# Performance work log

Hardware: AMD Instinct MI355X
Metric: run time of the kernel (lower is better)

Reference implementation:

```python
import jax, jax.numpy as jnp
import numpy as np

S, B, E = 2048, 2, 1024
H = 16
HD = E // H
RANK = 8
ALPHA = 16.0
LORA_SCALE = ALPHA / RANK


def setup_inputs() -> dict:
    key = jax.random.key(0)
    ks = jax.random.split(key, 13)
    d = {
        'query': jax.random.normal(ks[0], (S, B, E), jnp.float32),
        'key': jax.random.normal(ks[1], (S, B, E), jnp.float32),
        'value': jax.random.normal(ks[2], (S, B, E), jnp.float32),
        'in_proj_weight': jax.random.normal(ks[3], (3 * E, E), jnp.float32) * 0.02,
        'in_proj_bias': jax.random.normal(ks[4], (3 * E,), jnp.float32) * 0.02,
        'out_w': jax.random.normal(ks[5], (E, E), jnp.float32) * 0.02,
        'out_b': jax.random.normal(ks[6], (E,), jnp.float32) * 0.02,
        'A_q': jax.random.normal(ks[7], (RANK, E), jnp.float32) * 0.02,
        'B_q': jax.random.normal(ks[8], (E, RANK), jnp.float32) * 0.02,
        'A_k': jax.random.normal(ks[9], (RANK, E), jnp.float32) * 0.02,
        'B_k': jax.random.normal(ks[10], (E, RANK), jnp.float32) * 0.02,
        'A_v': jax.random.normal(ks[11], (RANK, E), jnp.float32) * 0.02,
        'B_v': jax.random.normal(ks[12], (E, RANK), jnp.float32) * 0.02,
    }
    return d


def _proj(x, W, b, A, Bm):
    # frozen linear + LoRA low-rank delta: x @ W.T + b + ((x @ A.T) @ B.T) * scale
    base = jnp.einsum('sbe,fe->sbf', x, W) + b
    lora = jnp.einsum('sbr,fr->sbf', jnp.einsum('sbe,re->sbr', x, A), Bm) * LORA_SCALE
    return base + lora


def reference(query, key, value, in_proj_weight, in_proj_bias, out_w, out_b,
              A_q, B_q, A_k, B_k, A_v, B_v):
    Wq, Wk, Wv = in_proj_weight[:E], in_proj_weight[E:2 * E], in_proj_weight[2 * E:]
    bq, bk, bv = in_proj_bias[:E], in_proj_bias[E:2 * E], in_proj_bias[2 * E:]
    q = _proj(query, Wq, bq, A_q, B_q)   # [S,B,E]
    k = _proj(key, Wk, bk, A_k, B_k)
    v = _proj(value, Wv, bv, A_v, B_v)
    # reshape to [B*H, S, HD] (seq-first layout, matching torch view/transpose)
    def heads(x):
        return x.reshape(S, B * H, HD).transpose(1, 0, 2)
    qh, kh, vh = heads(q), heads(k), heads(v)
    scale = HD ** -0.5
    attn = jnp.einsum('nsd,ntd->nst', qh, kh) * scale  # [B*H,S,S]
    attn = jax.nn.softmax(attn, axis=-1)
    out = jnp.einsum('nst,ntd->nsd', attn, vh)         # [B*H,S,HD]
    out = out.transpose(1, 0, 2).reshape(S, B, E)
    out = jnp.einsum('sbe,fe->sbf', out, out_w) + out_b
    return out
```

## Files before the change

kernel.cpp:

```cpp
#include <hip/hip_runtime.h>
#include <stdint.h>

static const int S_ = 2048, B_ = 2, E_ = 1024, H_ = 16, HD_ = 64, MR_ = 4096;

typedef __bf16 bf16;
typedef __bf16 bf16x8 __attribute__((ext_vector_type(8)));
typedef float  f32x4  __attribute__((ext_vector_type(4)));
typedef float  f32x16 __attribute__((ext_vector_type(16)));
typedef unsigned short u16x8 __attribute__((ext_vector_type(8)));

#define AS1(p) ((const __attribute__((address_space(1))) void*)(p))
#define AS3(p) ((__attribute__((address_space(3))) void*)(p))

#define QSCALE 0.18033688011112042f

static __device__ __forceinline__ uint32_t cvtpk_bf16(float lo, float hi) {
    uint32_t r;
    asm("v_cvt_pk_bf16_f32 %0, %1, %2" : "=v"(r) : "v"(lo), "v"(hi));
    return r;
}

__global__ __launch_bounds__(256) void prep_all(const float* __restrict__ s0,
                                                const float* __restrict__ s1,
                                                const float* __restrict__ s2,
                                                const float* __restrict__ s3,
                                                bf16* __restrict__ d0,
                                                bf16* __restrict__ d1,
                                                bf16* __restrict__ d2,
                                                bf16* __restrict__ d3,
                                                const float* __restrict__ W,
                                                const float* __restrict__ A0,
                                                const float* __restrict__ B0,
                                                const float* __restrict__ A1,
                                                const float* __restrict__ B1,
                                                const float* __restrict__ A2,
                                                const float* __restrict__ B2,
                                                bf16* __restrict__ o0,
                                                bf16* __restrict__ o1,
                                                bf16* __restrict__ o2) {
    int b = blockIdx.x;
    if (b < 6656) {
        const float* src;
        bf16* dst;
        int i;
        if (b < 6144) {
            int seg = b >> 11;
            i = (b & 2047) * 256 + threadIdx.x;
            src = seg == 0 ? s0 : (seg == 1 ? s1 : s2);
            dst = seg == 0 ? d0 : (seg == 1 ? d1 : d2);
        } else {
            i = (b - 6144) * 256 + threadIdx.x;
            src = s3; dst = d3;
        }
        const float4* s = (const float4*)src;
        float4 a = s[i * 2], c = s[i * 2 + 1];
        bf16x8 v;
        v[0] = (bf16)a.x; v[1] = (bf16)a.y; v[2] = (bf16)a.z; v[3] = (bf16)a.w;
        v[4] = (bf16)c.x; v[5] = (bf16)c.y; v[6] = (bf16)c.z; v[7] = (bf16)c.w;
        *(bf16x8*)(dst + (size_t)i * 8) = v;
    } else {
        int bb = b - 6656;
        int z = bb >> 12;
        const float* A = z == 0 ? A0 : (z == 1 ? A1 : A2);
        const float* Bm = z == 0 ? B0 : (z == 1 ? B1 : B2);
        bf16* out = z == 0 ? o0 : (z == 1 ? o1 : o2);
        const float* Wz = W + (size_t)z * 1024 * 1024;
        int idx = (bb & 4095) * 256 + threadIdx.x;
        int f = idx >> 10, e = idx & 1023;
        float acc = Wz[idx];
#pragma unroll
        for (int r = 0; r < 8; r++) acc += 2.0f * Bm[f * 8 + r] * A[r * 1024 + e];
        out[idx] = (bf16)acc;
    }
}

__global__ __launch_bounds__(256) void gemm_qkv(const bf16* __restrict__ XQ,
                                                const bf16* __restrict__ XK,
                                                const bf16* __restrict__ XV,
                                                const bf16* __restrict__ WQ,
                                                const bf16* __restrict__ WK,
                                                const bf16* __restrict__ WV,
                                                const float* __restrict__ ipb,
                                                bf16* __restrict__ QH,
                                                bf16* __restrict__ KH,
                                                bf16* __restrict__ VH) {
    int z = blockIdx.z;
    const bf16* Amat = z == 0 ? XQ : (z == 1 ? XK : XV);
    const bf16* Bmat = z == 0 ? WQ : (z == 1 ? WK : WV);
    bf16* Cout = z == 0 ? QH : (z == 1 ? KH : VH);
    const float* bias = ipb + z * 1024;
    float cscale = z == 0 ? QSCALE : 1.0f;

    __shared__ bf16 smbuf[16896];
    const int tid = threadIdx.x;
    const int wid = tid >> 6, lane = tid & 63;
    const int lg = lane >> 4, li = lane & 15;
    const int bidl = blockIdx.y * 8 + blockIdx.x;
    const int orig = (bidl & 7) * 32 + (bidl >> 3);
    const int m0 = (orig >> 3) * 128, n0 = (orig & 7) * 128;
    const int wr = wid >> 1, wc = wid & 1;

    f32x4 acc[4][4] = {};

    for (int kt = 0; kt < 1024; kt += 64) {
        __syncthreads();
#pragma unroll
        for (int h = 0; h < 2; h++)
#pragma unroll
            for (int i = 0; i < 2; i++) {
                int c = wid * 2 + i;
                const bf16* ga = Amat + (size_t)(m0 + c * 16 + (lane >> 2)) * 1024 + kt + h * 32 + (lane & 3) * 8;
                __builtin_amdgcn_global_load_lds(AS1(ga), AS3(smbuf + h * 4096 + c * 512), 16, 0, 0);
                const bf16* gb = Bmat + (size_t)(n0 + c * 16 + (lane >> 2)) * 1024 + kt + h * 32 + (lane & 3) * 8;
                __builtin_amdgcn_global_load_lds(AS1(gb), AS3(smbuf + 8192 + h * 4096 + c * 512), 16, 0, 0);
            }
        __syncthreads();

#pragma unroll
        for (int h = 0; h < 2; h++) {
            bf16x8 a[4], b[4];
#pragma unroll
            for (int mi = 0; mi < 4; mi++)
                a[mi] = *(const bf16x8*)(smbuf + h * 4096 + (wr * 64 + mi * 16 + li) * 32 + lg * 8);
#pragma unroll
            for (int ni = 0; ni < 4; ni++)
                b[ni] = *(const bf16x8*)(smbuf + 8192 + h * 4096 + (wc * 64 + ni * 16 + li) * 32 + lg * 8);
#pragma unroll
            for (int mi = 0; mi < 4; mi++)
#pragma unroll
                for (int ni = 0; ni < 4; ni++)
                    acc[mi][ni] = __builtin_amdgcn_mfma_f32_16x16x32_bf16(a[mi], b[ni], acc[mi][ni], 0, 0, 0);
        }
    }

    __syncthreads();
#pragma unroll
    for (int ni = 0; ni < 4; ni++) {
        int fl = wc * 64 + ni * 16 + li;
        float bv = bias[n0 + fl];
#pragma unroll
        for (int mi = 0; mi < 4; mi++)
#pragma unroll
            for (int r = 0; r < 4; r++) {
                int ml_ = wr * 64 + mi * 16 + lg * 4 + r;
                smbuf[ml_ * 132 + fl] = (bf16)((acc[mi][ni][r] + bv) * cscale);
            }
    }
    __syncthreads();
#pragma unroll
    for (int k = 0; k < 8; k++) {
        int c = tid + 256 * k;
        int dhalf = c & 7, m = (c >> 3) & 127, hl = c >> 10;
        u16x8 v = *(const u16x8*)(smbuf + m * 132 + hl * 64 + dhalf * 8);
        int mg = m0 + m, fg = n0 + hl * 64;
        int s = mg >> 1, bb = mg & 1, h = fg >> 6, d = dhalf * 8;
        *(u16x8*)(Cout + (size_t)(bb * 16 + h) * S_ * 64 + (size_t)s * 64 + d) = v;
    }
}

__global__ __launch_bounds__(256) void gemm_out64(const bf16* __restrict__ Amat,
                                                  const bf16* __restrict__ Bmat,
                                                  const float* __restrict__ bias,
                                                  float* __restrict__ Cout) {
    __shared__ bf16 Asm[2][64 * 32];
    __shared__ bf16 Bsm[2][128 * 32];
    const int tid = threadIdx.x;
    const int wid = tid >> 6, lane = tid & 63;
    const int lg = lane >> 4, li = lane & 15;
    const int bidl = blockIdx.y * 8 + blockIdx.x;
    const int orig = (bidl & 7) * 64 + (bidl >> 3);
    const int m0 = (orig >> 3) * 64, n0 = (orig & 7) * 128;
    const int wr = wid >> 1, wc = wid & 1;

    f32x4 acc[2][4] = {};

    for (int kt = 0; kt < 1024; kt += 64) {
        __syncthreads();
#pragma unroll
        for (int h = 0; h < 2; h++)
            for (int j = wid; j < 12; j += 4) {
                if (j < 4) {
                    const bf16* ga = Amat + (size_t)(m0 + j * 16 + (lane >> 2)) * 1024 + kt + h * 32 + (lane & 3) * 8;
                    __builtin_amdgcn_global_load_lds(AS1(ga), AS3(&Asm[h][j * 512]), 16, 0, 0);
                } else {
                    int c = j - 4;
                    const bf16* gb = Bmat + (size_t)(n0 + c * 16 + (lane >> 2)) * 1024 + kt + h * 32 + (lane & 3) * 8;
                    __builtin_amdgcn_global_load_lds(AS1(gb), AS3(&Bsm[h][c * 512]), 16, 0, 0);
                }
            }
        __syncthreads();

#pragma unroll
        for (int h = 0; h < 2; h++) {
            bf16x8 a[2], b[4];
#pragma unroll
            for (int mi = 0; mi < 2; mi++)
                a[mi] = *(const bf16x8*)(&Asm[h][(wr * 32 + mi * 16 + li) * 32 + lg * 8]);
#pragma unroll
            for (int ni = 0; ni < 4; ni++)
                b[ni] = *(const bf16x8*)(&Bsm[h][(wc * 64 + ni * 16 + li) * 32 + lg * 8]);
#pragma unroll
            for (int mi = 0; mi < 2; mi++)
#pragma unroll
                for (int ni = 0; ni < 4; ni++)
                    acc[mi][ni] = __builtin_amdgcn_mfma_f32_16x16x32_bf16(a[mi], b[ni], acc[mi][ni], 0, 0, 0);
        }
    }

#pragma unroll
    for (int ni = 0; ni < 4; ni++) {
        int f = n0 + wc * 64 + ni * 16 + li;
        float bv = bias[f];
#pragma unroll
        for (int mi = 0; mi < 2; mi++)
#pragma unroll
            for (int r = 0; r < 4; r++) {
                int m = m0 + wr * 32 + mi * 16 + lg * 4 + r;
                Cout[(size_t)m * 1024 + f] = acc[mi][ni][r] + bv;
            }
    }
}

__global__ __launch_bounds__(256, 4) void attn_fwd(const bf16* __restrict__ qh,
                                                   const bf16* __restrict__ kh,
                                                   const bf16* __restrict__ vh,
                                                   bf16* __restrict__ outbuf) {
    __shared__ __attribute__((aligned(16))) char smem[32768];

    const int bid = blockIdx.x;
    const int head = (bid & 7) * 4 + ((bid >> 3) & 3);
    const int qt = bid >> 5;
    const int tid = threadIdx.x, wid = tid >> 6, l = tid & 63;
    const int li = l & 31, hi = l >> 5;
    const int kvh = wid & 1;

    const bf16* Qb = qh + (size_t)head * S_ * 64;
    const bf16* Kb = kh + (size_t)head * S_ * 64;
    const bf16* Vb = vh + (size_t)head * S_ * 64;
    const int q0 = qt * 64 + (wid >> 1) * 32;

    bf16x8 qf[4];
#pragma unroll
    for (int s = 0; s < 4; s++)
        qf[s] = *(const bf16x8*)(Qb + (size_t)(q0 + li) * 64 + 16 * s + 8 * hi);

    f32x16 oacc0 = {}, oacc1 = {};
    float lsum = 0.f;

    const size_t kg_off = ((size_t)(16 * (l & 7)) ^ (16 * ((l >> 3) & 7)));
    const int vk2 = tid & 31, vdb = (tid >> 5) * 8;
    const int rswz = 16 * (li & 7);

#define STAGE_K(kv0, dstbuf)                                                    \
    {                                                                           \
        _Pragma("unroll")                                                       \
        for (int j = 0; j < 2; j++) {                                           \
            int row = (j * 4 + wid) * 8 + (l >> 3);                             \
            const char* srcp = (const char*)Kb + (size_t)((kv0) + row) * 128 + kg_off; \
            __builtin_amdgcn_global_load_lds(AS1(srcp),                         \
                AS3((dstbuf) + (j * 4 + wid) * 1024), 16, 0, 0);                \
        }                                                                       \
    }

    u16x8 vreg0, vreg1;
    vreg0 = *(const u16x8*)(Vb + (size_t)(2 * vk2) * 64 + vdb);
    vreg1 = *(const u16x8*)(Vb + (size_t)(2 * vk2 + 1) * 64 + vdb);
    STAGE_K(0, smem);

    for (int t = 0; t < 32; t++) {
        const int cur = t & 1;
        char* Kc = smem + cur * 8192;
        char* Vc = smem + 16384 + cur * 8192;
#pragma unroll
        for (int i = 0; i < 8; i++) {
            uint32_t w = (uint32_t)vreg0[i] | ((uint32_t)vreg1[i] << 16);
            *(uint32_t*)(Vc + (vdb + i) * 128 + ((4 * vk2) ^ (16 * i))) = w;
        }
        __syncthreads();
        if (t + 1 < 32) {
            int kv0 = (t + 1) * 64;
            vreg0 = *(const u16x8*)(Vb + (size_t)(kv0 + 2 * vk2) * 64 + vdb);
            vreg1 = *(const u16x8*)(Vb + (size_t)(kv0 + 2 * vk2 + 1) * 64 + vdb);
            STAGE_K(kv0, smem + (cur ^ 1) * 8192);
        }

        f32x16 s = {};
        __builtin_amdgcn_s_setprio(1);
#pragma unroll
        for (int step = 0; step < 4; step++) {
            bf16x8 k0 = *(const bf16x8*)(Kc + (kvh * 32 + li) * 128 + ((32 * step + 16 * hi) ^ rswz));
            s = __builtin_amdgcn_mfma_f32_32x32x16_bf16(k0, qf[step], s, 0, 0, 0);
        }
        __builtin_amdgcn_s_setprio(0);

        float p[16];
#pragma unroll
        for (int r = 0; r < 16; r++) p[r] = __builtin_amdgcn_exp2f(s[r]);
        lsum += (((p[0] + p[1]) + (p[2] + p[3])) + ((p[4] + p[5]) + (p[6] + p[7]))) +
                (((p[8] + p[9]) + (p[10] + p[11])) + ((p[12] + p[13]) + (p[14] + p[15])));

        bf16x8 pa[2];
#pragma unroll
        for (int st = 0; st < 2; st++) {
            uint32_t a0 = cvtpk_bf16(p[8 * st + 0], p[8 * st + 1]);
            uint32_t a1 = cvtpk_bf16(p[8 * st + 2], p[8 * st + 3]);
            uint32_t b0 = cvtpk_bf16(p[8 * st + 4], p[8 * st + 5]);
            uint32_t b1 = cvtpk_bf16(p[8 * st + 6], p[8 * st + 7]);
            asm("v_permlane32_swap_b32 %0, %1" : "+v"(a0), "+v"(b0));
            asm("v_permlane32_swap_b32 %0, %1" : "+v"(a1), "+v"(b1));
            union { uint32_t u[4]; bf16x8 v; } pu;
            pu.u[0] = a0; pu.u[1] = a1; pu.u[2] = b0; pu.u[3] = b1;
            pa[st] = pu.v;
        }

        __builtin_amdgcn_s_setprio(1);
#pragma unroll
        for (int st = 0; st < 2; st++) {
            int byteoff = (64 * kvh + 32 * st + 16 * hi) ^ rswz;
            bf16x8 v0 = *(const bf16x8*)(Vc + li * 128 + byteoff);
            oacc0 = __builtin_amdgcn_mfma_f32_32x32x16_bf16(pa[st], v0, oacc0, 0, 0, 0);
            bf16x8 v1 = *(const bf16x8*)(Vc + (32 + li) * 128 + byteoff);
            oacc1 = __builtin_amdgcn_mfma_f32_32x32x16_bf16(pa[st], v1, oacc1, 0, 0, 0);
        }
        __builtin_amdgcn_s_setprio(0);
    }

    __syncthreads();
    float* mlp = (float*)(smem + 16384);
    float* scr = (float*)smem;
    float lt = lsum + __shfl_xor(lsum, 32);
    if (l < 32) mlp[wid * 32 + l] = lt;
    {
        float* mys = scr + wid * 1024;
#pragma unroll
        for (int r = 0; r < 16; r++) {
            int rp = (r & 3) + 8 * (r >> 2) + 4 * hi;
            mys[rp * 32 + li] = kvh ? oacc0[r] : oacc1[r];
        }
    }
    __syncthreads();
    float pl = mlp[(wid ^ 1) * 32 + li];
    float linv = 1.0f / (lt + pl);
    const float* ps = scr + (wid ^ 1) * 1024;
    int bb = head >> 4, h = head & 15;
#pragma unroll
    for (int r = 0; r < 16; r++) {
        int rp = (r & 3) + 8 * (r >> 2) + 4 * hi;
        int q = q0 + rp;
        float own = kvh ? oacc1[r] : oacc0[r];
        float part = ps[rp * 32 + li];
        float val = (own + part) * __shfl(linv, rp);
        outbuf[(size_t)(q * 2 + bb) * 1024 + h * 64 + kvh * 32 + li] = (bf16)val;
    }
}

extern "C" void kernel_launch(void* const* d_in, const int* in_sizes, int n_in,
                              void* d_out, int out_size, void* d_ws, size_t ws_size,
                              hipStream_t stream) {
    const float* query = (const float*)d_in[0];
    const float* key_  = (const float*)d_in[1];
    const float* value = (const float*)d_in[2];
    const float* ipw   = (const float*)d_in[3];
    const float* ipb   = (const float*)d_in[4];
    const float* out_w = (const float*)d_in[5];
    const float* out_b = (const float*)d_in[6];
    const float* A_q   = (const float*)d_in[7];
    const float* B_q   = (const float*)d_in[8];
    const float* A_k   = (const float*)d_in[9];
    const float* B_k   = (const float*)d_in[10];
    const float* A_v   = (const float*)d_in[11];
    const float* B_v   = (const float*)d_in[12];

    const size_t MB = 1ull << 20;
    if (ws_size < 64 * MB) return;
    char* ws = (char*)d_ws;
    bf16* XQ = (bf16*)(ws + 0 * MB);
    bf16* XK = (bf16*)(ws + 8 * MB);
    bf16* XV = (bf16*)(ws + 16 * MB);
    bf16* WQ = (bf16*)(ws + 24 * MB);
    bf16* WK = (bf16*)(ws + 26 * MB);
    bf16* WV = (bf16*)(ws + 28 * MB);
    bf16* WO = (bf16*)(ws + 30 * MB);
    bf16* QH = (bf16*)(ws + 32 * MB);
    bf16* KH = (bf16*)(ws + 40 * MB);
    bf16* VH = (bf16*)(ws + 48 * MB);
    bf16* AT = (bf16*)(ws + 56 * MB);

    prep_all<<<18944, 256, 0, stream>>>(query, key_, value, out_w, XQ, XK, XV, WO,
                                        ipw, A_q, B_q, A_k, B_k, A_v, B_v,
                                        WQ, WK, WV);

    gemm_qkv<<<dim3(8, 32, 3), 256, 0, stream>>>(XQ, XK, XV, WQ, WK, WV, ipb, QH, KH, VH);

    attn_fwd<<<1024, 256, 0, stream>>>(QH, KH, VH, AT);

    gemm_out64<<<dim3(8, 64), 256, 0, stream>>>(AT, WO, out_b, (float*)d_out);
}
```

Measured before the change: 126.9 us.

## Fuse fp32-to-bf16 activation conversion into QKV GEMM tile loads

Removes the separate pass that converted query/key/value from fp32 to bf16 in the prep kernel. The QKV GEMM now streams fp32 activations directly into LDS, using an XOR swizzle against bank conflicts, and converts them to bf16 with packed conversion instructions when loading MFMA fragments. This avoids writing and re-reading the bf16 copies (about 48MB of traffic) and shrinks the prep kernel. In exchange the GEMM reads twice the A bytes per tile, uses 48KB of LDS (which may lower occupancy), and adds conversion instructions to the inner loop.

```diff
diff --git a/kernel.cpp b/kernel.cpp
--- a/kernel.cpp
+++ b/kernel.cpp
@@ -20,13 +20,7 @@
     return r;
 }
 
-__global__ __launch_bounds__(256) void prep_all(const float* __restrict__ s0,
-                                                const float* __restrict__ s1,
-                                                const float* __restrict__ s2,
-                                                const float* __restrict__ s3,
-                                                bf16* __restrict__ d0,
-                                                bf16* __restrict__ d1,
-                                                bf16* __restrict__ d2,
+__global__ __launch_bounds__(256) void prep_all(const float* __restrict__ s3,
                                                 bf16* __restrict__ d3,
                                                 const float* __restrict__ W,
                                                 const float* __restrict__ A0,
@@ -39,27 +33,16 @@
                                                 bf16* __restrict__ o1,
                                                 bf16* __restrict__ o2) {
     int b = blockIdx.x;
-    if (b < 6656) {
-        const float* src;
-        bf16* dst;
-        int i;
-        if (b < 6144) {
-            int seg = b >> 11;
-            i = (b & 2047) * 256 + threadIdx.x;
-            src = seg == 0 ? s0 : (seg == 1 ? s1 : s2);
-            dst = seg == 0 ? d0 : (seg == 1 ? d1 : d2);
-        } else {
-            i = (b - 6144) * 256 + threadIdx.x;
-            src = s3; dst = d3;
-        }
-        const float4* s = (const float4*)src;
+    if (b < 512) {
+        int i = b * 256 + threadIdx.x;
+        const float4* s = (const float4*)s3;
         float4 a = s[i * 2], c = s[i * 2 + 1];
         bf16x8 v;
         v[0] = (bf16)a.x; v[1] = (bf16)a.y; v[2] = (bf16)a.z; v[3] = (bf16)a.w;
         v[4] = (bf16)c.x; v[5] = (bf16)c.y; v[6] = (bf16)c.z; v[7] = (bf16)c.w;
-        *(bf16x8*)(dst + (size_t)i * 8) = v;
+        *(bf16x8*)(d3 + (size_t)i * 8) = v;
     } else {
-        int bb = b - 6656;
+        int bb = b - 512;
         int z = bb >> 12;
         const float* A = z == 0 ? A0 : (z == 1 ? A1 : A2);
         const float* Bm = z == 0 ? B0 : (z == 1 ? B1 : B2);
@@ -74,9 +57,9 @@
     }
 }
 
-__global__ __launch_bounds__(256) void gemm_qkv(const bf16* __restrict__ XQ,
-                                                const bf16* __restrict__ XK,
-                                                const bf16* __restrict__ XV,
+__global__ __launch_bounds__(256) void gemm_qkv(const float* __restrict__ Xq,
+                                                const float* __restrict__ Xk,
+                                                const float* __restrict__ Xv,
                                                 const bf16* __restrict__ WQ,
                                                 const bf16* __restrict__ WK,
                                                 const bf16* __restrict__ WV,
@@ -85,13 +68,13 @@
                                                 bf16* __restrict__ KH,
                                                 bf16* __restrict__ VH) {
     int z = blockIdx.z;
-    const bf16* Amat = z == 0 ? XQ : (z == 1 ? XK : XV);
+    const float* Amat = z == 0 ? Xq : (z == 1 ? Xk : Xv);
     const bf16* Bmat = z == 0 ? WQ : (z == 1 ? WK : WV);
     bf16* Cout = z == 0 ? QH : (z == 1 ? KH : VH);
     const float* bias = ipb + z * 1024;
     float cscale = z == 0 ? QSCALE : 1.0f;
 
-    __shared__ bf16 smbuf[16896];
+    __shared__ __attribute__((aligned(16))) char smem[49152];
     const int tid = threadIdx.x;
     const int wid = tid >> 6, lane = tid & 63;
     const int lg = lane >> 4, li = lane & 15;
@@ -102,29 +85,50 @@
 
     f32x4 acc[4][4] = {};
 
+    const int arow8 = lane >> 3;
+    const int asrc = ((lane & 7) ^ arow8) * 4;
+
     for (int kt = 0; kt < 1024; kt += 64) {
         __syncthreads();
 #pragma unroll
-        for (int h = 0; h < 2; h++)
+        for (int h = 0; h < 2; h++) {
+#pragma unroll
+            for (int i = 0; i < 4; i++) {
+                int c = wid * 4 + i;
+                int row = c * 8 + arow8;
+                const float* ga = Amat + (size_t)(m0 + row) * 1024 + kt + h * 32 + asrc;
+                __builtin_amdgcn_global_load_lds(AS1(ga), AS3(smem + h * 16384 + c * 1024), 16, 0, 0);
+            }
 #pragma unroll
             for (int i = 0; i < 2; i++) {
                 int c = wid * 2 + i;
-                const bf16* ga = Amat + (size_t)(m0 + c * 16 + (lane >> 2)) * 1024 + kt + h * 32 + (lane & 3) * 8;
-                __builtin_amdgcn_global_load_lds(AS1(ga), AS3(smbuf + h * 4096 + c * 512), 16, 0, 0);
                 const bf16* gb = Bmat + (size_t)(n0 + c * 16 + (lane >> 2)) * 1024 + kt + h * 32 + (lane & 3) * 8;
-                __builtin_amdgcn_global_load_lds(AS1(gb), AS3(smbuf + 8192 + h * 4096 + c * 512), 16, 0, 0);
-            }
+                __builtin_amdgcn_global_load_lds(AS1(gb), AS3(smem + 32768 + h * 8192 + c * 1024), 16, 0, 0);
+            }
+        }
         __syncthreads();
 
 #pragma unroll
         for (int h = 0; h < 2; h++) {
+            const char* Ab = smem + h * 16384;
+            const bf16* Bb = (const bf16*)(smem + 32768 + h * 8192);
             bf16x8 a[4], b[4];
 #pragma unroll
-            for (int mi = 0; mi < 4; mi++)
-                a[mi] = *(const bf16x8*)(smbuf + h * 4096 + (wr * 64 + mi * 16 + li) * 32 + lg * 8);
+            for (int mi = 0; mi < 4; mi++) {
+                int row = wr * 64 + mi * 16 + li;
+                int sx = (li & 7) * 16;
+                f32x4 lo = *(const f32x4*)(Ab + row * 128 + ((lg * 32) ^ sx));
+                f32x4 hi = *(const f32x4*)(Ab + row * 128 + ((lg * 32 + 16) ^ sx));
+                union { uint32_t u[4]; bf16x8 v; } au;
+                au.u[0] = cvtpk_bf16(lo[0], lo[1]);
+                au.u[1] = cvtpk_bf16(lo[2], lo[3]);
+                au.u[2] = cvtpk_bf16(hi[0], hi[1]);
+                au.u[3] = cvtpk_bf16(hi[2], hi[3]);
+                a[mi] = au.v;
+            }
 #pragma unroll
             for (int ni = 0; ni < 4; ni++)
-                b[ni] = *(const bf16x8*)(smbuf + 8192 + h * 4096 + (wc * 64 + ni * 16 + li) * 32 + lg * 8);
+                b[ni] = *(const bf16x8*)(Bb + (wc * 64 + ni * 16 + li) * 32 + lg * 8);
 #pragma unroll
             for (int mi = 0; mi < 4; mi++)
 #pragma unroll
@@ -134,6 +138,7 @@
     }
 
     __syncthreads();
+    bf16* smbuf = (bf16*)smem;
 #pragma unroll
     for (int ni = 0; ni < 4; ni++) {
         int fl = wc * 64 + ni * 16 + li;
@@ -374,9 +379,6 @@
     const size_t MB = 1ull << 20;
     if (ws_size < 64 * MB) return;
     char* ws = (char*)d_ws;
-    bf16* XQ = (bf16*)(ws + 0 * MB);
-    bf16* XK = (bf16*)(ws + 8 * MB);
-    bf16* XV = (bf16*)(ws + 16 * MB);
     bf16* WQ = (bf16*)(ws + 24 * MB);
     bf16* WK = (bf16*)(ws + 26 * MB);
     bf16* WV = (bf16*)(ws + 28 * MB);
@@ -386,11 +388,11 @@
     bf16* VH = (bf16*)(ws + 48 * MB);
     bf16* AT = (bf16*)(ws + 56 * MB);
 
-    prep_all<<<18944, 256, 0, stream>>>(query, key_, value, out_w, XQ, XK, XV, WO,
-                                        ipw, A_q, B_q, A_k, B_k, A_v, B_v,
+    prep_all<<<12800, 256, 0, stream>>>(out_w, WO, ipw, A_q, B_q, A_k, B_k, A_v, B_v,
                                         WQ, WK, WV);
 
-    gemm_qkv<<<dim3(8, 32, 3), 256, 0, stream>>>(XQ, XK, XV, WQ, WK, WV, ipb, QH, KH, VH);
+    gemm_qkv<<<dim3(8, 32, 3), 256, 0, stream>>>(query, key_, value, WQ, WK, WV,
+                                                 ipb, QH, KH, VH);
 
     attn_fwd<<<1024, 256, 0, stream>>>(QH, KH, VH, AT);
 
```

After: 134.4 us. +5.9%, slower.
